# Kernel tuning notes

Measured on AMD Instinct MI355X. Metric: run time of the kernel, lower is better.

## Reference

```python
import jax, jax.numpy as jnp
import numpy as np

R = 3           # disp_range = (3, 3)
DU = 2 * R + 1  # 7 displacements per axis, 49 total
PNAMES = ['mn_w1','mn_b1','mn_w2','mn_b2','mn_w3','mn_b3','mn_w4','mn_b4','mn_wd','mn_bd','mn_w5','mn_b5','dap_w','dap_b','me_w1','me_b1','me_w2','me_b2','me_w3','me_b3','gz1_w','gz1_b','gr1_w','gr1_b','gq1_w','gq1_b','gz2_w','gz2_b','gr2_w','gr2_b','gq2_w','gq2_b','fh_w1','fh_b1','fh_w2','fh_b2']


def conv2d(x, w, b, stride=(1, 1), padding=((1, 1), (1, 1))):
    y = jax.lax.conv_general_dilated(x, w, stride, padding, dimension_numbers=('NCHW', 'OIHW', 'NCHW'))
    return y + b[None, :, None, None]


def warp_backwards(f, flow):
    # bilinear backward warp with zero padding; flow[:,0]=u (x offset), flow[:,1]=v (y offset)
    B, C, H, W = f.shape
    gy, gx = jnp.meshgrid(jnp.arange(H, dtype=flow.dtype), jnp.arange(W, dtype=flow.dtype), indexing='ij')
    x = gx[None] + flow[:, 0]
    y = gy[None] + flow[:, 1]
    x0, y0 = jnp.floor(x), jnp.floor(y)
    wx, wy = x - x0, y - y0

    def corner(yy, xx, wgt):
        valid = (yy >= 0) & (yy <= H - 1) & (xx >= 0) & (xx <= W - 1)
        yc = jnp.clip(yy, 0, H - 1).astype(jnp.int32)
        xc = jnp.clip(xx, 0, W - 1).astype(jnp.int32)
        g = jax.vmap(lambda fb, yb, xb: fb[:, yb, xb])(f, yc, xc)  # (B,C,H,W)
        return g * (wgt * valid.astype(f.dtype))[:, None]

    return (corner(y0, x0, (1 - wy) * (1 - wx)) + corner(y0, x0 + 1, (1 - wy) * wx)
            + corner(y0 + 1, x0, wy * (1 - wx)) + corner(y0 + 1, x0 + 1, wy * wx))


def gru_step(h, x, wz, bz, wr, br, wq, bq, pad):
    hx = jnp.concatenate([h, x], axis=1)
    z = jax.nn.sigmoid(conv2d(hx, wz, bz, padding=pad))
    r = jax.nn.sigmoid(conv2d(hx, wr, br, padding=pad))
    q = jnp.tanh(conv2d(jnp.concatenate([r * h, x], axis=1), wq, bq, padding=pad))
    return (1.0 - z) * h + z * q


def _run(fmap1, fmap2, h, flow, P):
    B, C, H, W = fmap1.shape
    lrelu, relu = jax.nn.leaky_relu, jax.nn.relu
    # backward warp of fmap2 by current (detached) flow
    f2w = warp_backwards(fmap2, jax.lax.stop_gradient(flow))
    # --- correlation volume: 49 zero-padded shifts of warped fmap2, paired with fmap1 ---
    pad2 = jnp.pad(f2w, ((0, 0), (0, 0), (R, R), (R, R)))
    # k = i*DU + j  <->  shift (di, dj) = (i-R, j-R); shifted[...,y,x] = f2w[y+dj, x+di]
    shifted = jnp.stack([pad2[:, :, j:j + H, i:i + W] for i in range(DU) for j in range(DU)], axis=1)  # (B,49,C,H,W)
    valid = (jnp.sum(shifted, axis=2, keepdims=True) != 0).astype(fmap1.dtype)
    mvol = jnp.concatenate([jnp.broadcast_to(fmap1[:, None], shifted.shape), shifted], axis=2) * valid  # (B,49,2C,H,W)
    # --- matching net, applied per displacement ---
    x = mvol.reshape(B * DU * DU, 2 * C, H, W)
    x = relu(conv2d(x, P['mn_w1'], P['mn_b1']))
    x = relu(conv2d(x, P['mn_w2'], P['mn_b2'], stride=(2, 2)))
    x = relu(conv2d(x, P['mn_w3'], P['mn_b3']))
    x = relu(conv2d(x, P['mn_w4'], P['mn_b4']))
    # ConvTranspose2d(k=4, s=2, p=1) == lhs-dilated conv with pad 2
    x = jax.lax.conv_general_dilated(x, P['mn_wd'], (1, 1), ((2, 2), (2, 2)), lhs_dilation=(2, 2), dimension_numbers=('NCHW', 'OIHW', 'NCHW')) + P['mn_bd'][None, :, None, None]
    x = relu(x)
    x = conv2d(x, P['mn_w5'], P['mn_b5'])  # (B*49, 1, H, W)
    cvol = x.reshape(B, DU * DU, H, W)
    # --- displacement-aware projection: 1x1 conv across the 49 displacement channels ---
    cvol = jnp.einsum('ok,bkhw->bohw', P['dap_w'], cvol) + P['dap_b'][None, :, None, None]
    # --- motion encoder ---
    m = jnp.concatenate([cvol, fmap1, flow], axis=1)  # (B, 49+C+2, H, W)
    m = lrelu(conv2d(m, P['me_w1'], P['me_b1']))
    m = lrelu(conv2d(m, P['me_w2'], P['me_b2']))
    m = conv2d(m, P['me_w3'], P['me_b3'])             # (B, 94, H, W)
    xg = jnp.concatenate([m, flow], axis=1)           # (B, 96, H, W)
    # --- separable conv GRU: horizontal (1x5) then vertical (5x1) pass ---
    h = gru_step(h, xg, P['gz1_w'], P['gz1_b'], P['gr1_w'], P['gr1_b'], P['gq1_w'], P['gq1_b'], ((0, 0), (2, 2)))
    h = gru_step(h, xg, P['gz2_w'], P['gz2_b'], P['gr2_w'], P['gr2_b'], P['gq2_w'], P['gq2_b'], ((2, 2), (0, 0)))
    # --- flow head: softmax over 49 displacements, expectation of displacement grid ---
    s = lrelu(jnp.einsum('oi,bihw->bohw', P['fh_w1'], h) + P['fh_b1'][None, :, None, None])
    s = lrelu(jnp.einsum('oi,bihw->bohw', P['fh_w2'], s) + P['fh_b2'][None, :, None, None])
    prob = jax.nn.softmax(s, axis=1)  # (B, 49, H, W)
    dr = jnp.arange(-R, R + 1, dtype=fmap1.dtype)
    disp = jnp.stack([jnp.broadcast_to(dr[:, None], (DU, DU)), jnp.broadcast_to(dr[None, :], (DU, DU))], axis=0).reshape(2, DU * DU)
    d = jnp.einsum('bkhw,ck->bchw', prob, disp)
    return h, flow + d


def _params(key):
    shapes = {'mn_w1': (96, 64, 3, 3), 'mn_b1': (96,), 'mn_w2': (128, 96, 3, 3), 'mn_b2': (128,), 'mn_w3': (128, 128, 3, 3), 'mn_b3': (128,), 'mn_w4': (64, 128, 3, 3), 'mn_b4': (64,), 'mn_wd': (32, 64, 4, 4), 'mn_bd': (32,), 'mn_w5': (1, 32, 3, 3), 'mn_b5': (1,), 'dap_w': (49, 49), 'dap_b': (49,), 'me_w1': (128, 83, 3, 3), 'me_b1': (128,), 'me_w2': (128, 128, 3, 3), 'me_b2': (128,), 'me_w3': (94, 128, 3, 3), 'me_b3': (94,), 'gz1_w': (128, 224, 1, 5), 'gz1_b': (128,), 'gr1_w': (128, 224, 1, 5), 'gr1_b': (128,), 'gq1_w': (128, 224, 1, 5), 'gq1_b': (128,), 'gz2_w': (128, 224, 5, 1), 'gz2_b': (128,), 'gr2_w': (128, 224, 5, 1), 'gr2_b': (128,), 'gq2_w': (128, 224, 5, 1), 'gq2_b': (128,), 'fh_w1': (256, 128), 'fh_b1': (256,), 'fh_w2': (49, 256), 'fh_b2': (49,)}
    keys = jax.random.split(key, len(shapes))
    return {n: jax.random.normal(k, s, dtype=jnp.float32) * 0.05 for (n, s), k in zip(shapes.items(), keys)}


def setup_inputs():
    key = jax.random.key(0)
    k1, k2, k3, k4, kp = jax.random.split(key, 5)
    B, C, H, W, HID = 2, 32, 64, 96, 128
    inp = {'fmap1': jax.random.normal(k1, (B, C, H, W), jnp.float32),
           'fmap2': jax.random.normal(k2, (B, C, H, W), jnp.float32),
           'h': jax.random.normal(k3, (B, HID, H, W), jnp.float32),
           'flow': jax.random.normal(k4, (B, 2, H, W), jnp.float32),
           'i': 0}
    inp.update(_params(kp))
    return inp


def reference(fmap1, fmap2, h, flow, mn_w1, mn_b1, mn_w2, mn_b2, mn_w3, mn_b3, mn_w4, mn_b4, mn_wd, mn_bd, mn_w5, mn_b5, dap_w, dap_b, me_w1, me_b1, me_w2, me_b2, me_w3, me_b3, gz1_w, gz1_b, gr1_w, gr1_b, gq1_w, gq1_b, gz2_w, gz2_b, gr2_w, gr2_b, gq2_w, gq2_b, fh_w1, fh_b1, fh_w2, fh_b2, i):
    ps = (mn_w1, mn_b1, mn_w2, mn_b2, mn_w3, mn_b3, mn_w4, mn_b4, mn_wd, mn_bd, mn_w5, mn_b5, dap_w, dap_b, me_w1, me_b1, me_w2, me_b2, me_w3, me_b3, gz1_w, gz1_b, gr1_w, gr1_b, gq1_w, gq1_b, gz2_w, gz2_b, gr2_w, gr2_b, gq2_w, gq2_b, fh_w1, fh_b1, fh_w2, fh_b2)
    return _run(fmap1, fmap2, h, flow, dict(zip(PNAMES, ps)))
```

## Files before the change

kernel.cpp:

```cpp
#include <hip/hip_runtime.h>
#include <math.h>

typedef unsigned short u16;
typedef unsigned int u32;
typedef __attribute__((ext_vector_type(8))) short bf16x8;
typedef __attribute__((ext_vector_type(4))) float f32x4;

#define HWW 6144

__device__ __forceinline__ float sigmoidf_(float x) { return 1.f / (1.f + expf(-x)); }
__device__ __forceinline__ float lrelu_(float x) { return x >= 0.f ? x : 0.01f * x; }
__device__ __forceinline__ u16 f2bf(float f) {
    u32 u = __float_as_uint(f);
    u += 0x7fffu + ((u >> 16) & 1u);
    return (u16)(u >> 16);
}
__device__ __forceinline__ float bf2f(u16 h) { return __uint_as_float(((u32)h) << 16); }
__device__ __forceinline__ u32 pk2(float a, float b) { return (u32)f2bf(a) | ((u32)f2bf(b) << 16); }

struct WJob { const float* src; unsigned long dstOff; int OC, rowOff, IC, ICP, NT; unsigned long cum; };
struct WJobs { WJob j[16]; long total; };

__global__ __launch_bounds__(256) void k_wt_all(WJobs J, u16* __restrict__ base)
{
    long i = (long)blockIdx.x * 256 + threadIdx.x;
    if (i >= J.total) return;
    int jb = 0;
    #pragma unroll
    for (int k = 1; k < 16; ++k) if (i >= (long)J.j[k].cum) jb = k;
    WJob w = J.j[jb];
    long local = i - (long)w.cum;
    int c = (int)(local % w.ICP);
    int t = (int)((local / w.ICP) % w.NT);
    int o = (int)(local / ((long)w.ICP * w.NT));
    float val = (c < w.IC) ? w.src[((long)o * w.IC + c) * w.NT + t] : 0.f;
    base[w.dstOff + ((long)(w.rowOff + o) * w.NT + t) * w.ICP + c] = f2bf(val);
}

__global__ __launch_bounds__(256) void k_wt_dq(const float* __restrict__ w, u16* __restrict__ dst)
{
    int i = blockIdx.x * 256 + threadIdx.x;
    if (i >= 32768) return;
    int c = i & 63; int t = (i >> 6) & 3; int o = (i >> 8) & 31; int q = i >> 13;
    int ry = q >> 1, rx = q & 1, ta = t >> 1, tb = t & 1;
    int ky = ry + 2 * ta, kx = rx + 2 * tb;
    float val = w[(((long)o * 64 + c) * 4 + ky) * 4 + kx];
    dst[(long)q * 8192 + o * 256 + t * 64 + c] = f2bf(val);
}

__global__ __launch_bounds__(256) void k_wt5(const float* __restrict__ w, float* __restrict__ wt)
{
    int i = blockIdx.x * 256 + threadIdx.x;
    if (i >= 288) return;
    int t = i % 9, c = i / 9;
    wt[t * 32 + c] = w[c * 9 + t];
}

__global__ void k_catb(const float* __restrict__ a, const float* __restrict__ b, float* __restrict__ d)
{
    int i = threadIdx.x;
    if (i < 128) d[i] = a[i];
    else if (i < 256) d[i] = b[i - 128];
}

__global__ __launch_bounds__(256) void k_prep_f1(const float* __restrict__ fmap1, u16* __restrict__ f1bf)
{
    int gid = blockIdx.x * 256 + threadIdx.x;
    if (gid >= 24576) return;
    int idx = gid >> 1, half = gid & 1;
    int b = idx / HWW, p = idx % HWW;
    const float* fb = fmap1 + (long)b * 32 * HWW + p + (long)(half * 16) * HWW;
    u32 pk[8];
    #pragma unroll
    for (int c2 = 0; c2 < 8; ++c2)
        pk[c2] = pk2(fb[(long)(2 * c2) * HWW], fb[(long)(2 * c2 + 1) * HWW]);
    u16* op = f1bf + ((long)idx << 5) + half * 16;
    ((uint4*)op)[0] = make_uint4(pk[0], pk[1], pk[2], pk[3]);
    ((uint4*)op)[1] = make_uint4(pk[4], pk[5], pk[6], pk[7]);
}

__global__ __launch_bounds__(256) void k_warp(const float* __restrict__ fmap2, const float* __restrict__ flow,
                                              u16* __restrict__ f2wbf, float* __restrict__ cs)
{
    int gid = blockIdx.x * 256 + threadIdx.x;
    if (gid >= 24576) return;
    int idx = gid >> 1, half = gid & 1;
    int b = idx / HWW, p = idx % HWW, y = p / 96, x = p % 96;
    float u = flow[(b * 2 + 0) * HWW + p], v = flow[(b * 2 + 1) * HWW + p];
    float fx = (float)x + u, fy = (float)y + v;
    float fx0 = floorf(fx), fy0 = floorf(fy);
    float wx = fx - fx0, wy = fy - fy0;
    int x0 = (int)fx0, y0i = (int)fy0, x1 = x0 + 1, y1 = y0i + 1;
    bool vx0 = x0 >= 0 && x0 < 96, vx1 = x1 >= 0 && x1 < 96;
    bool vy0 = y0i >= 0 && y0i < 64, vy1 = y1 >= 0 && y1 < 64;
    float m00 = (vy0 && vx0) ? (1.f - wy) * (1.f - wx) : 0.f;
    float m01 = (vy0 && vx1) ? (1.f - wy) * wx : 0.f;
    float m10 = (vy1 && vx0) ? wy * (1.f - wx) : 0.f;
    float m11 = (vy1 && vx1) ? wy * wx : 0.f;
    int cx0 = min(max(x0, 0), 95), cx1 = min(max(x1, 0), 95);
    int cy0 = min(max(y0i, 0), 63), cy1 = min(max(y1, 0), 63);
    int i00 = cy0 * 96 + cx0, i01 = cy0 * 96 + cx1, i10 = cy1 * 96 + cx0, i11 = cy1 * 96 + cx1;
    const float* fb = fmap2 + (long)b * 32 * HWW + (long)(half * 16) * HWW;
    float s = 0.f; u32 pk[8];
    #pragma unroll
    for (int c2 = 0; c2 < 8; ++c2) {
        const float* fa = fb + (long)(2 * c2) * HWW;
        const float* fc = fb + (long)(2 * c2 + 1) * HWW;
        float g0 = m00 * fa[i00] + m01 * fa[i01] + m10 * fa[i10] + m11 * fa[i11];
        float g1 = m00 * fc[i00] + m01 * fc[i01] + m10 * fc[i10] + m11 * fc[i11];
        s += g0 + g1;
        pk[c2] = pk2(g0, g1);
    }
    u16* op = f2wbf + ((long)idx << 5) + half * 16;
    ((uint4*)op)[0] = make_uint4(pk[0], pk[1], pk[2], pk[3]);
    ((uint4*)op)[1] = make_uint4(pk[4], pk[5], pk[6], pk[7]);
    float stot = s + __shfl_xor(s, 1);
    if (half == 0) cs[idx] = stot;
}

template<int BN, int MODE, int KH, int KW, int PH, int PW, int STRIDE, int ACT, int OUTF32,
         int IH, int IW, int OH, int OW, int ICP, int NKT>
__global__ __launch_bounds__(256) void k_gemm(
    const u16* __restrict__ A0, const u16* __restrict__ A1,
    const float* __restrict__ csm, const u16* __restrict__ Wb,
    const float* __restrict__ bias,
    u16* __restrict__ outb, u16* __restrict__ outb2, float* __restrict__ outf,
    int OC, int ldc, int coff, int nOff)
{
    constexpr int WAVES_M = (BN == 128) ? 2 : 4;
    constexpr int WTM = 128 / WAVES_M;
    constexpr int WTN = (BN == 128) ? 64 : BN;
    constexpr int MF = WTM / 16;
    constexpr int NF = WTN / 16;
    constexpr int LDR = 40;
    __shared__ u16 As[2][128 * LDR];
    __shared__ u16 Bs[2][BN * LDR];
    int tid = threadIdx.x;
    int mrow = tid >> 1;
    int khOff = (tid & 1) << 4;
    int gmS = blockIdx.x * 128 + mrow;

    constexpr int OHW = (MODE == 1) ? 6144 : ((MODE == 2) ? 1536 : OH * OW);
    constexpr int OWW = (MODE == 1) ? 96 : ((MODE == 2) ? 48 : OW);
    int nImg = gmS / OHW;
    int rem = gmS - nImg * OHW;
    int y0 = rem / OWW, x0 = rem - y0 * OWW;

    int ryz = 0, rxz = 0, diS = 0, djS = 0, bImgHWW = 0;
    u32 vmask = 0;
    const u16* Arow = A0;
    if (MODE == 0) {
        Arow = A0 + ((long)nImg * IH * IW + (long)y0 * STRIDE * IW + (long)x0 * STRIDE) * ICP + khOff;
    } else if (MODE == 1) {
        int n = nOff + nImg;
        int bImg = n / 49; int kd = n - bImg * 49;
        diS = kd / 7 - 3; djS = kd % 7 - 3;
        bImgHWW = bImg * HWW;
        #pragma unroll
        for (int t = 0; t < 9; ++t) {
            int dy = t / 3 - 1, dx = t % 3 - 1;
            int yy = y0 + dy, xx = x0 + dx, ys = yy + djS, xs = xx + diS;
            bool v = yy >= 0 && yy < 64 && xx >= 0 && xx < 96 && ys >= 0 && ys < 64 && xs >= 0 && xs < 96;
            if (v) v = (csm[bImgHWW + ys * 96 + xs] != 0.f);
            vmask |= (v ? 1u : 0u) << t;
        }
    } else {
        ryz = blockIdx.z >> 1; rxz = blockIdx.z & 1;
    }
    const u16* WbZ = Wb + (MODE == 2 ? (long)blockIdx.z * 32 * 256 : 0);
    int n0 = blockIdx.y * BN;

    auto loadTile = [&](int kt, uint4& va0, uint4& va1) {
        va0 = make_uint4(0u, 0u, 0u, 0u); va1 = make_uint4(0u, 0u, 0u, 0u);
        if (MODE == 0) {
            constexpr int KTC = ICP / 32;
            int t = kt / KTC;
            int c0 = (kt - t * KTC) << 5;
            int dy = t / KW - PH, dx = t - (t / KW) * KW - PW;
            int iy = y0 * STRIDE + dy, ix = x0 * STRIDE + dx;
            if (iy >= 0 && iy < IH && ix >= 0 && ix < IW) {
                const u16* sp = Arow + (long)(dy * IW + dx) * ICP + c0;
                va0 = *(const uint4*)sp; va1 = *(const uint4*)(sp + 8);
            }
        } else if (MODE == 1) {
            int t = kt >> 1, half = kt & 1;
            if ((vmask >> t) & 1u) {
                int dy = t / 3 - 1, dx = t % 3 - 1;
                int yy = y0 + dy, xx = x0 + dx;
                const u16* sp = half ? (A1 + (((long)bImgHWW + (yy + djS) * 96 + (xx + diS)) << 5) + khOff)
                                     : (A0 + (((long)bImgHWW + yy * 96 + xx) << 5) + khOff);
                va0 = *(const uint4*)sp; va1 = *(const uint4*)(sp + 8);
            }
        } else {
            int t = kt >> 1, c0 = (kt & 1) << 5;
            int ta = t >> 1, tb = t & 1;
            int iy = y0 + ryz + ta - 1, ix = x0 + rxz + tb - 1;
            if (iy >= 0 && iy < 32 && ix >= 0 && ix < 48) {
                const u16* sp = A0 + (((long)(nImg * 32 + iy) * 48 + ix) << 6) + c0 + khOff;
                va0 = *(const uint4*)sp; va1 = *(const uint4*)(sp + 8);
            }
        }
    };

    int lane = tid & 63, wid = tid >> 6;
    int wm = (BN == 128) ? (wid >> 1) : wid;
    int wn = (BN == 128) ? (wid & 1) : 0;
    int fr = lane & 15, fg = lane >> 4;
    f32x4 acc[MF][NF];
    #pragma unroll
    for (int i = 0; i < MF; ++i)
        #pragma unroll
        for (int j = 0; j < NF; ++j)
            acc[i][j] = (f32x4){0.f, 0.f, 0.f, 0.f};

    bool bldr = (tid < 2 * BN);
    int brow = tid >> 1, ko = (tid & 1) << 4;
    const u16* Bp = WbZ + (long)(n0 + brow) * (NKT * 32) + ko;

    {
        uint4 a0c, a1c;
        loadTile(0, a0c, a1c);
        *(uint4*)&As[0][mrow * LDR + khOff] = a0c;
        *(uint4*)&As[0][mrow * LDR + khOff + 8] = a1c;
        if (bldr) {
            *(uint4*)&Bs[0][brow * LDR + ko] = *(const uint4*)Bp;
            *(uint4*)&Bs[0][brow * LDR + ko + 8] = *(const uint4*)(Bp + 8);
        }
    }
    __syncthreads();

    #pragma unroll
    for (int kt = 0; kt < NKT; ++kt) {
        constexpr int last = NKT - 1;
        int cur = kt & 1;
        uint4 na0, na1, nb0, nb1;
        if (kt < last) {
            loadTile(kt + 1, na0, na1);
            if (bldr) {
                const u16* wp = Bp + (long)(kt + 1) * 32;
                nb0 = *(const uint4*)wp; nb1 = *(const uint4*)(wp + 8);
            }
        }
        bf16x8 af[MF], bfv[NF];
        #pragma unroll
        for (int i = 0; i < MF; ++i)
            af[i] = *(const bf16x8*)&As[cur][(wm * WTM + i * 16 + fr) * LDR + fg * 8];
        #pragma unroll
        for (int j = 0; j < NF; ++j)
            bfv[j] = *(const bf16x8*)&Bs[cur][(wn * WTN + j * 16 + fr) * LDR + fg * 8];
        #pragma unroll
        for (int i = 0; i < MF; ++i)
            #pragma unroll
            for (int j = 0; j < NF; ++j)
                acc[i][j] = __builtin_amdgcn_mfma_f32_16x16x32_bf16(af[i], bfv[j], acc[i][j], 0, 0, 0);
        if (kt < last) {
            int bufn = cur ^ 1;
            *(uint4*)&As[bufn][mrow * LDR + khOff] = na0;
            *(uint4*)&As[bufn][mrow * LDR + khOff + 8] = na1;
            if (bldr) {
                *(uint4*)&Bs[bufn][brow * LDR + ko] = nb0;
                *(uint4*)&Bs[bufn][brow * LDR + ko + 8] = nb1;
            }
            __syncthreads();
        }
    }

    #pragma unroll
    for (int i = 0; i < MF; ++i) {
        #pragma unroll
        for (int j = 0; j < NF; ++j) {
            int nn = n0 + wn * WTN + j * 16 + fr;
            if (nn >= OC) continue;
            #pragma unroll
            for (int rr = 0; rr < 4; ++rr) {
                int mloc = wm * WTM + i * 16 + fg * 4 + rr;
                long gm = (long)blockIdx.x * 128 + mloc;
                float v = acc[i][j][rr] + bias[nn];
                if (ACT == 1) v = fmaxf(v, 0.f);
                else if (ACT == 2) v = lrelu_(v);
                if (OUTF32) {
                    outf[gm * ldc + coff + nn] = v;
                } else if (MODE == 2) {
                    int nI = (int)(gm / 1536); int rq = (int)(gm - (long)nI * 1536);
                    int Y = rq / 48, X = rq - (rq / 48) * 48;
                    long di = (((long)nI * 64 + 2 * Y + ryz) * 96 + (2 * X + rxz)) * 32 + nn;
                    outb[di] = f2bf(v);
                } else {
                    long di = gm * ldc + coff + nn;
                    u16 hv = f2bf(v);
                    outb[di] = hv;
                    if (outb2) outb2[di] = hv;
                }
            }
        }
    }
}

__global__ __launch_bounds__(256) void k_conv5n(const u16* __restrict__ x5, const float* __restrict__ w5t,
                                                const float* __restrict__ b5, u16* __restrict__ cvolT,
                                                int N, int n0)
{
    int idx = blockIdx.x * 256 + threadIdx.x;
    if (idx >= N * HWW) return;
    int nl = idx / HWW, p = idx % HWW, y = p / 96, x = p % 96;
    float acc = b5[0];
    #pragma unroll
    for (int t = 0; t < 9; ++t) {
        int iy = y + t / 3 - 1, ix = x + t % 3 - 1;
        if (iy < 0 || iy >= 64 || ix < 0 || ix >= 96) continue;
        const u16* sp = x5 + (((long)nl * HWW + iy * 96 + ix) << 5);
        const float* wt_ = w5t + t * 32;
        #pragma unroll
        for (int c8 = 0; c8 < 4; ++c8) {
            uint4 v = *(const uint4*)(sp + c8 * 8);
            acc = fmaf(bf2f((u16)(v.x & 0xffffu)), wt_[c8 * 8 + 0], acc);
            acc = fmaf(bf2f((u16)(v.x >> 16)),     wt_[c8 * 8 + 1], acc);
            acc = fmaf(bf2f((u16)(v.y & 0xffffu)), wt_[c8 * 8 + 2], acc);
            acc = fmaf(bf2f((u16)(v.y >> 16)),     wt_[c8 * 8 + 3], acc);
            acc = fmaf(bf2f((u16)(v.z & 0xffffu)), wt_[c8 * 8 + 4], acc);
            acc = fmaf(bf2f((u16)(v.z >> 16)),     wt_[c8 * 8 + 5], acc);
            acc = fmaf(bf2f((u16)(v.w & 0xffffu)), wt_[c8 * 8 + 6], acc);
            acc = fmaf(bf2f((u16)(v.w >> 16)),     wt_[c8 * 8 + 7], acc);
        }
    }
    int n = n0 + nl;
    int b = n / 49, k = n - b * 49;
    cvolT[((long)b * HWW + p) * 64 + k] = f2bf(acc);
}

__global__ __launch_bounds__(256) void k_me_tail(const float* __restrict__ fmap1, const float* __restrict__ flow,
                                                 u16* __restrict__ mein)
{
    int gid = blockIdx.x * 256 + threadIdx.x;
    if (gid >= 73728) return;
    int j = gid / 12288, idx = gid - j * 12288;
    int b = idx / HWW, p = idx % HWW;
    int c0 = 49 + j * 8;
    u16* mp = mein + (long)idx * 96;
    #pragma unroll
    for (int q = 0; q < 8; ++q) {
        int c = c0 + q;
        if (c >= 96) break;
        float v;
        if (c < 81) v = fmap1[((long)(b * 32 + (c - 49))) * HWW + p];
        else if (c == 81) v = flow[(b * 2 + 0) * HWW + p];
        else if (c == 82) v = flow[(b * 2 + 1) * HWW + p];
        else v = 0.f;
        mp[c] = f2bf(v);
    }
}

__global__ __launch_bounds__(256) void k_set_head(const float* __restrict__ h, const float* __restrict__ flow,
                                                  float* __restrict__ hst, u16* __restrict__ hx,
                                                  u16* __restrict__ hx2)
{
    int gid = blockIdx.x * 256 + threadIdx.x;
    if (gid >= 49152) return;
    int cq = gid / 12288, idx = gid - cq * 12288;
    int b = idx / HWW, p = idx % HWW;
    int c0 = cq * 32;
    const float* hp = h + (long)b * 128 * HWW + p;
    float* hs = hst + (long)idx * 128;
    u16* hxp = hx + (long)idx * 224;
    #pragma unroll
    for (int c = c0; c < c0 + 32; c += 8) {
        float v[8];
        #pragma unroll
        for (int q = 0; q < 8; ++q) v[q] = hp[(long)(c + q) * HWW];
        *(float4*)&hs[c] = make_float4(v[0], v[1], v[2], v[3]);
        *(float4*)&hs[c + 4] = make_float4(v[4], v[5], v[6], v[7]);
        uint4 pk = make_uint4(pk2(v[0], v[1]), pk2(v[2], v[3]), pk2(v[4], v[5]), pk2(v[6], v[7]));
        *(uint4*)&hxp[c] = pk;
    }
    if (cq == 0) {
        u16 uu = f2bf(flow[(b * 2 + 0) * HWW + p]);
        u16 vv = f2bf(flow[(b * 2 + 1) * HWW + p]);
        long o = (long)idx * 224;
        hx[o + 222] = uu; hx[o + 223] = vv;
        hx2[o + 222] = uu; hx2[o + 223] = vv;
    }
}

__global__ __launch_bounds__(256) void k_post_zr(const float* __restrict__ azr, const float* __restrict__ hst,
                                                 float* __restrict__ z, u16* __restrict__ hx2)
{
    int gid = blockIdx.x * 256 + threadIdx.x;
    if (gid >= 49152) return;
    int cq = gid / 12288, idx = gid - cq * 12288;
    int c0 = cq * 32;
    const float* ap = azr + (long)idx * 256;
    const float* hs = hst + (long)idx * 128;
    float* zp = z + (long)idx * 128;
    u16* xp = hx2 + (long)idx * 224;
    #pragma unroll
    for (int c = c0; c < c0 + 32; c += 8) {
        float4 a0 = *(const float4*)&ap[c], a1 = *(const float4*)&ap[c + 4];
        float4 r0 = *(const float4*)&ap[128 + c], r1 = *(const float4*)&ap[128 + c + 4];
        float4 h0 = *(const float4*)&hs[c], h1v = *(const float4*)&hs[c + 4];
        float z0 = sigmoidf_(a0.x), z1 = sigmoidf_(a0.y), z2 = sigmoidf_(a0.z), z3 = sigmoidf_(a0.w);
        float z4 = sigmoidf_(a1.x), z5 = sigmoidf_(a1.y), z6 = sigmoidf_(a1.z), z7 = sigmoidf_(a1.w);
        *(float4*)&zp[c] = make_float4(z0, z1, z2, z3);
        *(float4*)&zp[c + 4] = make_float4(z4, z5, z6, z7);
        float rh0 = sigmoidf_(r0.x) * h0.x, rh1 = sigmoidf_(r0.y) * h0.y;
        float rh2 = sigmoidf_(r0.z) * h0.z, rh3 = sigmoidf_(r0.w) * h0.w;
        float rh4 = sigmoidf_(r1.x) * h1v.x, rh5 = sigmoidf_(r1.y) * h1v.y;
        float rh6 = sigmoidf_(r1.z) * h1v.z, rh7 = sigmoidf_(r1.w) * h1v.w;
        uint4 pk = make_uint4(pk2(rh0, rh1), pk2(rh2, rh3), pk2(rh4, rh5), pk2(rh6, rh7));
        *(uint4*)&xp[c] = pk;
    }
}

template<int FIN>
__global__ __launch_bounds__(256) void k_post_q(const float* __restrict__ aq, const float* __restrict__ z,
                                                const float* __restrict__ hst, float* __restrict__ h1f,
                                                u16* __restrict__ hxdst, float* __restrict__ outH)
{
    int gid = blockIdx.x * 256 + threadIdx.x;
    if (gid >= 49152) return;
    int cq = gid / 12288, idx = gid - cq * 12288;
    int b = idx / HWW, p = idx % HWW;
    int c0 = cq * 32;
    const float* ap = aq + (long)idx * 128;
    const float* zp = z + (long)idx * 128;
    const float* hs = hst + (long)idx * 128;
    #pragma unroll
    for (int c = c0; c < c0 + 32; c += 8) {
        float hn[8];
        #pragma unroll
        for (int q = 0; q < 8; ++q) {
            float qq = tanhf(ap[c + q]);
            float zv = zp[c + q];
            hn[q] = (1.f - zv) * hs[c + q] + zv * qq;
        }
        uint4 pk = make_uint4(pk2(hn[0], hn[1]), pk2(hn[2], hn[3]), pk2(hn[4], hn[5]), pk2(hn[6], hn[7]));
        if (FIN == 0) {
            *(float4*)&h1f[(long)idx * 128 + c] = make_float4(hn[0], hn[1], hn[2], hn[3]);
            *(float4*)&h1f[(long)idx * 128 + c + 4] = make_float4(hn[4], hn[5], hn[6], hn[7]);
            *(uint4*)&hxdst[(long)idx * 224 + c] = pk;
        } else {
            #pragma unroll
            for (int q = 0; q < 8; ++q)
                outH[((long)(b * 128 + c + q)) * HWW + p] = hn[q];
            *(uint4*)&hxdst[(long)idx * 128 + c] = pk;
        }
    }
}

__global__ __launch_bounds__(256) void k_soft(const float* __restrict__ s2, const float* __restrict__ flow,
                                              float* __restrict__ outFlow)
{
    int idx = blockIdx.x * 256 + threadIdx.x;
    if (idx >= 12288) return;
    int b = idx / HWW, p = idx % HWW;
    const float* sp = s2 + (long)idx * 64;
    float lg[49];
    #pragma unroll
    for (int k = 0; k < 48; k += 4) {
        float4 v = *(const float4*)&sp[k];
        lg[k] = v.x; lg[k + 1] = v.y; lg[k + 2] = v.z; lg[k + 3] = v.w;
    }
    lg[48] = sp[48];
    float m = -1e30f;
    #pragma unroll
    for (int k = 0; k < 49; ++k) m = fmaxf(m, lg[k]);
    float s = 0.f, a0 = 0.f, a1 = 0.f;
    #pragma unroll
    for (int k = 0; k < 49; ++k) {
        float e = expf(lg[k] - m);
        s += e;
        a0 += e * (float)(k / 7 - 3);
        a1 += e * (float)(k % 7 - 3);
    }
    float inv = 1.f / s;
    outFlow[(long)(b * 2 + 0) * HWW + p] = flow[(long)(b * 2 + 0) * HWW + p] + a0 * inv;
    outFlow[(long)(b * 2 + 1) * HWW + p] = flow[(long)(b * 2 + 1) * HWW + p] + a1 * inv;
}

extern "C" void kernel_launch(void* const* d_in, const int* in_sizes, int n_in,
                              void* d_out, int out_size, void* d_ws, size_t ws_size,
                              hipStream_t stream)
{
    const float* fmap1 = (const float*)d_in[0];
    const float* fmap2 = (const float*)d_in[1];
    const float* h     = (const float*)d_in[2];
    const float* flow  = (const float*)d_in[3];
    int pb = (in_sizes[4] == 1) ? 5 : 4;
    const float* mn_w1 = (const float*)d_in[pb + 0];
    const float* mn_b1 = (const float*)d_in[pb + 1];
    const float* mn_w2 = (const float*)d_in[pb + 2];
    const float* mn_b2 = (const float*)d_in[pb + 3];
    const float* mn_w3 = (const float*)d_in[pb + 4];
    const float* mn_b3 = (const float*)d_in[pb + 5];
    const float* mn_w4 = (const float*)d_in[pb + 6];
    const float* mn_b4 = (const float*)d_in[pb + 7];
    const float* mn_wd = (const float*)d_in[pb + 8];
    const float* mn_bd = (const float*)d_in[pb + 9];
    const float* mn_w5 = (const float*)d_in[pb + 10];
    const float* mn_b5 = (const float*)d_in[pb + 11];
    const float* dap_w = (const float*)d_in[pb + 12];
    const float* dap_b = (const float*)d_in[pb + 13];
    const float* me_w1 = (const float*)d_in[pb + 14];
    const float* me_b1 = (const float*)d_in[pb + 15];
    const float* me_w2 = (const float*)d_in[pb + 16];
    const float* me_b2 = (const float*)d_in[pb + 17];
    const float* me_w3 = (const float*)d_in[pb + 18];
    const float* me_b3 = (const float*)d_in[pb + 19];
    const float* gz1_w = (const float*)d_in[pb + 20];
    const float* gz1_b = (const float*)d_in[pb + 21];
    const float* gr1_w = (const float*)d_in[pb + 22];
    const float* gr1_b = (const float*)d_in[pb + 23];
    const float* gq1_w = (const float*)d_in[pb + 24];
    const float* gq1_b = (const float*)d_in[pb + 25];
    const float* gz2_w = (const float*)d_in[pb + 26];
    const float* gz2_b = (const float*)d_in[pb + 27];
    const float* gr2_w = (const float*)d_in[pb + 28];
    const float* gr2_b = (const float*)d_in[pb + 29];
    const float* gq2_w = (const float*)d_in[pb + 30];
    const float* gq2_b = (const float*)d_in[pb + 31];
    const float* fh_w1 = (const float*)d_in[pb + 32];
    const float* fh_b1 = (const float*)d_in[pb + 33];
    const float* fh_w2 = (const float*)d_in[pb + 34];
    const float* fh_b2 = (const float*)d_in[pb + 35];

    char* wsB = (char*)d_ws;
    size_t off = 0;
    auto alc = [&](size_t bytes) { size_t o = off; off = (off + bytes + 255) & ~(size_t)255; return o; };

    size_t o_wc1  = alc(128 * 576 * 2);
    size_t o_wc2  = alc(128 * 864 * 2);
    size_t o_wc3  = alc((size_t)128 * 1152 * 2);
    size_t o_wc4  = alc((size_t)64 * 1152 * 2);
    size_t o_wdq  = alc(32768 * 2);
    size_t o_wme1 = alc(128 * 864 * 2);
    size_t o_wme2 = alc((size_t)128 * 1152 * 2);
    size_t o_wme3 = alc((size_t)128 * 1152 * 2);
    size_t o_wzr1 = alc((size_t)256 * 1120 * 2);
    size_t o_wq1  = alc((size_t)128 * 1120 * 2);
    size_t o_wzr2 = alc((size_t)256 * 1120 * 2);
    size_t o_wq2  = alc((size_t)128 * 1120 * 2);
    size_t o_wfh1 = alc(256 * 128 * 2);
    size_t o_wfh2 = alc(64 * 256 * 2);
    size_t o_wdapb= alc(64 * 64 * 2);
    size_t o_w5t  = alc(288 * 4);
    size_t o_bzr1 = alc(256 * 4);
    size_t o_bzr2 = alc(256 * 4);
    size_t wArenaBytes = off;

    size_t o_f1bf = alc((size_t)12288 * 32 * 2);
    size_t o_f2wb = alc((size_t)12288 * 32 * 2);
    size_t o_cs   = alc(12288 * 4);
    size_t o_cvolT= alc((size_t)12288 * 64 * 2);

    const int CH = 49;
    size_t sharedBase = off;
    size_t offA = sharedBase;
    auto alcA = [&](size_t bytes) { size_t o = offA; offA = (offA + bytes + 255) & ~(size_t)255; return o; };
    size_t o_x1 = alcA((size_t)CH * 6144 * 96 * 2);
    size_t o_x2 = alcA((size_t)98 * 1536 * 128 * 2);
    size_t o_x3 = alcA((size_t)98 * 1536 * 128 * 2);
    size_t o_x4 = alcA((size_t)98 * 1536 * 64 * 2);
    size_t o_x5 = alcA((size_t)98 * 6144 * 32 * 2);
    size_t offB2 = sharedBase;
    auto alcB = [&](size_t bytes) { size_t o = offB2; offB2 = (offB2 + bytes + 255) & ~(size_t)255; return o; };
    size_t o_mein = alcB((size_t)12288 * 96 * 2);
    size_t o_m1   = alcB((size_t)12288 * 128 * 2);
    size_t o_m2   = alcB((size_t)12288 * 128 * 2);
    size_t o_hx   = alcB((size_t)12288 * 224 * 2);
    size_t o_hx2  = alcB((size_t)12288 * 224 * 2);
    size_t o_h2bf = alcB((size_t)12288 * 128 * 2);
    size_t o_s1b  = alcB((size_t)12288 * 256 * 2);
    size_t o_hst  = alcB((size_t)12288 * 128 * 4);
    size_t o_h1f  = alcB((size_t)12288 * 128 * 4);
    size_t o_zf   = alcB((size_t)12288 * 128 * 4);
    size_t o_azr  = alcB((size_t)12288 * 256 * 4);
    size_t o_aqf  = alcB((size_t)12288 * 128 * 4);
    size_t o_s2   = alcB((size_t)12288 * 64 * 4);

    u16* wbase = (u16*)wsB;
    u16* wdq  = (u16*)(wsB + o_wdq);
    float* w5t = (float*)(wsB + o_w5t);
    float* bzr1 = (float*)(wsB + o_bzr1);
    float* bzr2 = (float*)(wsB + o_bzr2);
    u16* wc1  = (u16*)(wsB + o_wc1);   u16* wc2  = (u16*)(wsB + o_wc2);
    u16* wc3  = (u16*)(wsB + o_wc3);   u16* wc4  = (u16*)(wsB + o_wc4);
    u16* wme1 = (u16*)(wsB + o_wme1);  u16* wme2 = (u16*)(wsB + o_wme2);
    u16* wme3 = (u16*)(wsB + o_wme3);
    u16* wzr1 = (u16*)(wsB + o_wzr1);  u16* wq1  = (u16*)(wsB + o_wq1);
    u16* wzr2 = (u16*)(wsB + o_wzr2);  u16* wq2  = (u16*)(wsB + o_wq2);
    u16* wfh1 = (u16*)(wsB + o_wfh1);  u16* wfh2 = (u16*)(wsB + o_wfh2);
    u16* wdapb= (u16*)(wsB + o_wdapb);

    u16* f1bf = (u16*)(wsB + o_f1bf);  u16* f2wb = (u16*)(wsB + o_f2wb);
    float* cs = (float*)(wsB + o_cs);
    u16* cvolT = (u16*)(wsB + o_cvolT);
    u16* x1 = (u16*)(wsB + o_x1); u16* x2 = (u16*)(wsB + o_x2); u16* x3 = (u16*)(wsB + o_x3);
    u16* x4 = (u16*)(wsB + o_x4); u16* x5 = (u16*)(wsB + o_x5);
    u16* mein = (u16*)(wsB + o_mein);
    u16* m1 = (u16*)(wsB + o_m1); u16* m2 = (u16*)(wsB + o_m2);
    u16* hx = (u16*)(wsB + o_hx); u16* hx2 = (u16*)(wsB + o_hx2);
    u16* h2bf = (u16*)(wsB + o_h2bf);  u16* s1b = (u16*)(wsB + o_s1b);
    float* hst = (float*)(wsB + o_hst); float* h1f = (float*)(wsB + o_h1f);
    float* zf = (float*)(wsB + o_zf); float* azr = (float*)(wsB + o_azr);
    float* aqf = (float*)(wsB + o_aqf); float* s2 = (float*)(wsB + o_s2);

    float* outH = (float*)d_out;
    float* outFlow = outH + (long)2 * 128 * HWW;

    auto nb = [](long total, int bs) { return (unsigned)((total + bs - 1) / bs); };

    hipMemsetAsync(wsB, 0, wArenaBytes, stream);
    hipMemsetAsync(wsB + o_cvolT, 0, (size_t)12288 * 64 * 2, stream);

    WJobs J;
    {
        auto mk = [](const float* src, size_t dstOffBytes, int OC, int rowOff, int IC, int ICP, int NT) {
            WJob w; w.src = src; w.dstOff = dstOffBytes / 2; w.OC = OC; w.rowOff = rowOff;
            w.IC = IC; w.ICP = ICP; w.NT = NT; w.cum = 0; return w;
        };
        J.j[0]  = mk(mn_w1, o_wc1, 96, 0, 64, 64, 9);
        J.j[1]  = mk(mn_w2, o_wc2, 128, 0, 96, 96, 9);
        J.j[2]  = mk(mn_w3, o_wc3, 128, 0, 128, 128, 9);
        J.j[3]  = mk(mn_w4, o_wc4, 64, 0, 128, 128, 9);
        J.j[4]  = mk(me_w1, o_wme1, 128, 0, 83, 96, 9);
        J.j[5]  = mk(me_w2, o_wme2, 128, 0, 128, 128, 9);
        J.j[6]  = mk(me_w3, o_wme3, 94, 0, 128, 128, 9);
        J.j[7]  = mk(gz1_w, o_wzr1, 128, 0, 224, 224, 5);
        J.j[8]  = mk(gr1_w, o_wzr1, 128, 128, 224, 224, 5);
        J.j[9]  = mk(gq1_w, o_wq1, 128, 0, 224, 224, 5);
        J.j[10] = mk(gz2_w, o_wzr2, 128, 0, 224, 224, 5);
        J.j[11] = mk(gr2_w, o_wzr2, 128, 128, 224, 224, 5);
        J.j[12] = mk(gq2_w, o_wq2, 128, 0, 224, 224, 5);
        J.j[13] = mk(fh_w1, o_wfh1, 256, 0, 128, 128, 1);
        J.j[14] = mk(fh_w2, o_wfh2, 49, 0, 256, 256, 1);
        J.j[15] = mk(dap_w, o_wdapb, 49, 0, 49, 64, 1);
        long cum = 0;
        for (int k = 0; k < 16; ++k) {
            J.j[k].cum = cum;
            cum += (long)J.j[k].OC * J.j[k].NT * J.j[k].ICP;
        }
        J.total = cum;
    }
    k_wt_all<<<nb(J.total, 256), 256, 0, stream>>>(J, wbase);
    k_wt_dq<<<nb(32768, 256), 256, 0, stream>>>(mn_wd, wdq);
    k_wt5<<<2, 256, 0, stream>>>(mn_w5, w5t);
    k_catb<<<1, 256, 0, stream>>>(gz1_b, gr1_b, bzr1);
    k_catb<<<1, 256, 0, stream>>>(gz2_b, gr2_b, bzr2);

    k_prep_f1<<<nb(24576, 256), 256, 0, stream>>>(fmap1, f1bf);
    k_warp<<<nb(24576, 256), 256, 0, stream>>>(fmap2, flow, f2wb, cs);

    for (int n0 = 0; n0 < 98; n0 += CH) {
        k_gemm<128,1,3,3,1,1,1,1,0,64,96,64,96,32,18><<<dim3(2352, 1), 256, 0, stream>>>(
            f1bf, f2wb, cs, wc1, mn_b1, x1, nullptr, nullptr, 96, 96, 0, n0);
        k_gemm<128,0,3,3,1,1,2,1,0,64,96,32,48,96,27><<<dim3(588, 1), 256, 0, stream>>>(
            x1, nullptr, nullptr, wc2, mn_b2, x2 + (long)n0 * 196608, nullptr, nullptr, 128, 128, 0, 0);
    }
    k_gemm<128,0,3,3,1,1,1,1,0,32,48,32,48,128,36><<<dim3(1176, 1), 256, 0, stream>>>(
        x2, nullptr, nullptr, wc3, mn_b3, x3, nullptr, nullptr, 128, 128, 0, 0);
    k_gemm<64,0,3,3,1,1,1,1,0,32,48,32,48,128,36><<<dim3(1176, 1), 256, 0, stream>>>(
        x3, nullptr, nullptr, wc4, mn_b4, x4, nullptr, nullptr, 64, 64, 0, 0);
    k_gemm<32,2,4,4,2,2,1,1,0,32,48,32,48,64,8><<<dim3(1176, 1, 4), 256, 0, stream>>>(
        x4, nullptr, nullptr, wdq, mn_bd, x5, nullptr, nullptr, 32, 32, 0, 0);
    k_conv5n<<<nb(98L * HWW, 256), 256, 0, stream>>>(x5, w5t, mn_b5, cvolT, 98, 0);

    k_gemm<64,0,1,1,0,0,1,0,0,64,96,64,96,64,2><<<dim3(96, 1), 256, 0, stream>>>(
        cvolT, nullptr, nullptr, wdapb, dap_b, mein, nullptr, nullptr, 49, 96, 0, 0);
    k_me_tail<<<nb(73728, 256), 256, 0, stream>>>(fmap1, flow, mein);

    k_gemm<128,0,3,3,1,1,1,2,0,64,96,64,96,96,27><<<dim3(96, 1), 256, 0, stream>>>(
        mein, nullptr, nullptr, wme1, me_b1, m1, nullptr, nullptr, 128, 128, 0, 0);
    k_gemm<128,0,3,3,1,1,1,2,0,64,96,64,96,128,36><<<dim3(96, 1), 256, 0, stream>>>(
        m1, nullptr, nullptr, wme2, me_b2, m2, nullptr, nullptr, 128, 128, 0, 0);
    k_gemm<128,0,3,3,1,1,1,0,0,64,96,64,96,128,36><<<dim3(96, 1), 256, 0, stream>>>(
        m2, nullptr, nullptr, wme3, me_b3, hx, hx2, nullptr, 94, 224, 128, 0);

    k_set_head<<<nb(49152, 256), 256, 0, stream>>>(h, flow, hst, hx, hx2);
    k_gemm<128,0,1,5,0,2,1,0,1,64,96,64,96,224,35><<<dim3(96, 2), 256, 0, stream>>>(
        hx, nullptr, nullptr, wzr1, bzr1, nullptr, nullptr, azr, 256, 256, 0, 0);
    k_post_zr<<<nb(49152, 256), 256, 0, stream>>>(azr, hst, zf, hx2);
    k_gemm<128,0,1,5,0,2,1,0,1,64,96,64,96,224,35><<<dim3(96, 1), 256, 0, stream>>>(
        hx2, nullptr, nullptr, wq1, gq1_b, nullptr, nullptr, aqf, 128, 128, 0, 0);
    k_post_q<0><<<nb(49152, 256), 256, 0, stream>>>(aqf, zf, hst, h1f, hx, nullptr);

    k_gemm<128,0,5,1,2,0,1,0,1,64,96,64,96,224,35><<<dim3(96, 2), 256, 0, stream>>>(
        hx, nullptr, nullptr, wzr2, bzr2, nullptr, nullptr, azr, 256, 256, 0, 0);
    k_post_zr<<<nb(49152, 256), 256, 0, stream>>>(azr, h1f, zf, hx2);
    k_gemm<128,0,5,1,2,0,1,0,1,64,96,64,96,224,35><<<dim3(96, 1), 256, 0, stream>>>(
        hx2, nullptr, nullptr, wq2, gq2_b, nullptr, nullptr, aqf, 128, 128, 0, 0);
    k_post_q<1><<<nb(49152, 256), 256, 0, stream>>>(aqf, zf, h1f, nullptr, h2bf, outH);

    k_gemm<128,0,1,1,0,0,1,2,0,64,96,64,96,128,4><<<dim3(96, 2), 256, 0, stream>>>(
        h2bf, nullptr, nullptr, wfh1, fh_b1, s1b, nullptr, nullptr, 256, 256, 0, 0);
    k_gemm<64,0,1,1,0,0,1,2,1,64,96,64,96,256,8><<<dim3(96, 1), 256, 0, stream>>>(
        s1b, nullptr, nullptr, wfh2, fh_b2, nullptr, nullptr, s2, 49, 64, 0, 0);
    k_soft<<<nb(12288, 256), 256, 0, stream>>>(s2, flow, outFlow);
}
```

Baseline: 776.7 us.

## Add BM tile parameter and deepen global-load prefetch to two stages

Templates the GEMM kernel on the M tile size, so the small per-pixel convolutions in the motion encoder, GRU and flow head use 64-row tiles and launch twice as many blocks. It also restructures the main loop so global loads for tile k+2 are issued while tile k computes and tile k+1 is written to shared memory, hiding more load latency. The intent is better CU occupancy on the small launches and more latency hiding on all GEMMs. In exchange it holds extra prefetch registers per thread, which may reduce occupancy in the large correlation-stage GEMMs.

```diff
diff --git a/kernel.cpp b/kernel.cpp
--- a/kernel.cpp
+++ b/kernel.cpp
@@ -118,7 +118,7 @@
     if (half == 0) cs[idx] = stot;
 }
 
-template<int BN, int MODE, int KH, int KW, int PH, int PW, int STRIDE, int ACT, int OUTF32,
+template<int BM, int BN, int MODE, int KH, int KW, int PH, int PW, int STRIDE, int ACT, int OUTF32,
          int IH, int IW, int OH, int OW, int ICP, int NKT>
 __global__ __launch_bounds__(256) void k_gemm(
     const u16* __restrict__ A0, const u16* __restrict__ A1,
@@ -127,18 +127,20 @@
     u16* __restrict__ outb, u16* __restrict__ outb2, float* __restrict__ outf,
     int OC, int ldc, int coff, int nOff)
 {
-    constexpr int WAVES_M = (BN == 128) ? 2 : 4;
-    constexpr int WTM = 128 / WAVES_M;
-    constexpr int WTN = (BN == 128) ? 64 : BN;
+    constexpr int WAVES_M = (BM == 64) ? 2 : ((BN == 128) ? 2 : 4);
+    constexpr int WAVES_N = 4 / WAVES_M;
+    constexpr int WTM = BM / WAVES_M;
+    constexpr int WTN = BN / WAVES_N;
     constexpr int MF = WTM / 16;
     constexpr int NF = WTN / 16;
     constexpr int LDR = 40;
-    __shared__ u16 As[2][128 * LDR];
+    __shared__ u16 As[2][BM * LDR];
     __shared__ u16 Bs[2][BN * LDR];
     int tid = threadIdx.x;
-    int mrow = tid >> 1;
-    int khOff = (tid & 1) << 4;
-    int gmS = blockIdx.x * 128 + mrow;
+    constexpr int ATHR = 256 / BM;
+    int mrow = tid / ATHR;
+    int khOff = (tid % ATHR) * (32 / ATHR);
+    int gmS = blockIdx.x * BM + mrow;
 
     constexpr int OHW = (MODE == 1) ? 6144 : ((MODE == 2) ? 1536 : OH * OW);
     constexpr int OWW = (MODE == 1) ? 96 : ((MODE == 2) ? 48 : OW);
@@ -180,7 +182,8 @@
             int iy = y0 * STRIDE + dy, ix = x0 * STRIDE + dx;
             if (iy >= 0 && iy < IH && ix >= 0 && ix < IW) {
                 const u16* sp = Arow + (long)(dy * IW + dx) * ICP + c0;
-                va0 = *(const uint4*)sp; va1 = *(const uint4*)(sp + 8);
+                va0 = *(const uint4*)sp;
+                if (BM == 128) va1 = *(const uint4*)(sp + 8);
             }
         } else if (MODE == 1) {
             int t = kt >> 1, half = kt & 1;
@@ -189,7 +192,8 @@
                 int yy = y0 + dy, xx = x0 + dx;
                 const u16* sp = half ? (A1 + (((long)bImgHWW + (yy + djS) * 96 + (xx + diS)) << 5) + khOff)
                                      : (A0 + (((long)bImgHWW + yy * 96 + xx) << 5) + khOff);
-                va0 = *(const uint4*)sp; va1 = *(const uint4*)(sp + 8);
+                va0 = *(const uint4*)sp;
+                if (BM == 128) va1 = *(const uint4*)(sp + 8);
             }
         } else {
             int t = kt >> 1, c0 = (kt & 1) << 5;
@@ -197,49 +201,59 @@
             int iy = y0 + ryz + ta - 1, ix = x0 + rxz + tb - 1;
             if (iy >= 0 && iy < 32 && ix >= 0 && ix < 48) {
                 const u16* sp = A0 + (((long)(nImg * 32 + iy) * 48 + ix) << 6) + c0 + khOff;
-                va0 = *(const uint4*)sp; va1 = *(const uint4*)(sp + 8);
+                va0 = *(const uint4*)sp;
+                if (BM == 128) va1 = *(const uint4*)(sp + 8);
             }
         }
     };
-
-    int lane = tid & 63, wid = tid >> 6;
-    int wm = (BN == 128) ? (wid >> 1) : wid;
-    int wn = (BN == 128) ? (wid & 1) : 0;
-    int fr = lane & 15, fg = lane >> 4;
-    f32x4 acc[MF][NF];
-    #pragma unroll
-    for (int i = 0; i < MF; ++i)
-        #pragma unroll
-        for (int j = 0; j < NF; ++j)
-            acc[i][j] = (f32x4){0.f, 0.f, 0.f, 0.f};
+    auto writeA = [&](int bufn, const uint4& va0, const uint4& va1) {
+        *(uint4*)&As[bufn][mrow * LDR + khOff] = va0;
+        if (BM == 128) *(uint4*)&As[bufn][mrow * LDR + khOff + 8] = va1;
+    };
 
     bool bldr = (tid < 2 * BN);
     int brow = tid >> 1, ko = (tid & 1) << 4;
     const u16* Bp = WbZ + (long)(n0 + brow) * (NKT * 32) + ko;
-
+    auto loadB = [&](int kt, uint4& vb0, uint4& vb1) {
+        const u16* wp = Bp + (long)kt * 32;
+        vb0 = *(const uint4*)wp; vb1 = *(const uint4*)(wp + 8);
+    };
+    auto writeB = [&](int bufn, const uint4& vb0, const uint4& vb1) {
+        *(uint4*)&Bs[bufn][brow * LDR + ko] = vb0;
+        *(uint4*)&Bs[bufn][brow * LDR + ko + 8] = vb1;
+    };
+
+    int lane = tid & 63, wid = tid >> 6;
+    int wm = (WAVES_N == 2) ? (wid >> 1) : wid;
+    int wn = (WAVES_N == 2) ? (wid & 1) : 0;
+    int fr = lane & 15, fg = lane >> 4;
+    f32x4 acc[MF][NF];
+    #pragma unroll
+    for (int i = 0; i < MF; ++i)
+        #pragma unroll
+        for (int j = 0; j < NF; ++j)
+            acc[i][j] = (f32x4){0.f, 0.f, 0.f, 0.f};
+
+    uint4 pa0, pa1, pb0, pb1;
     {
-        uint4 a0c, a1c;
-        loadTile(0, a0c, a1c);
-        *(uint4*)&As[0][mrow * LDR + khOff] = a0c;
-        *(uint4*)&As[0][mrow * LDR + khOff + 8] = a1c;
-        if (bldr) {
-            *(uint4*)&Bs[0][brow * LDR + ko] = *(const uint4*)Bp;
-            *(uint4*)&Bs[0][brow * LDR + ko + 8] = *(const uint4*)(Bp + 8);
-        }
+        uint4 t0, t1;
+        loadTile(0, t0, t1);
+        writeA(0, t0, t1);
+        if (bldr) { uint4 u0, u1; loadB(0, u0, u1); writeB(0, u0, u1); }
+    }
+    if (NKT > 1) {
+        loadTile(1, pa0, pa1);
+        if (bldr) loadB(1, pb0, pb1);
     }
     __syncthreads();
 
     #pragma unroll
     for (int kt = 0; kt < NKT; ++kt) {
-        constexpr int last = NKT - 1;
         int cur = kt & 1;
-        uint4 na0, na1, nb0, nb1;
-        if (kt < last) {
-            loadTile(kt + 1, na0, na1);
-            if (bldr) {
-                const u16* wp = Bp + (long)(kt + 1) * 32;
-                nb0 = *(const uint4*)wp; nb1 = *(const uint4*)(wp + 8);
-            }
+        uint4 qa0, qa1, qb0, qb1;
+        if (kt + 2 < NKT) {
+            loadTile(kt + 2, qa0, qa1);
+            if (bldr) loadB(kt + 2, qb0, qb1);
         }
         bf16x8 af[MF], bfv[NF];
         #pragma unroll
@@ -253,15 +267,12 @@
             #pragma unroll
             for (int j = 0; j < NF; ++j)
                 acc[i][j] = __builtin_amdgcn_mfma_f32_16x16x32_bf16(af[i], bfv[j], acc[i][j], 0, 0, 0);
-        if (kt < last) {
+        if (kt + 1 < NKT) {
             int bufn = cur ^ 1;
-            *(uint4*)&As[bufn][mrow * LDR + khOff] = na0;
-            *(uint4*)&As[bufn][mrow * LDR + khOff + 8] = na1;
-            if (bldr) {
-                *(uint4*)&Bs[bufn][brow * LDR + ko] = nb0;
-                *(uint4*)&Bs[bufn][brow * LDR + ko + 8] = nb1;
-            }
+            writeA(bufn, pa0, pa1);
+            if (bldr) writeB(bufn, pb0, pb1);
             __syncthreads();
+            pa0 = qa0; pa1 = qa1; pb0 = qb0; pb1 = qb1;
         }
     }
 
@@ -274,7 +285,7 @@
             #pragma unroll
             for (int rr = 0; rr < 4; ++rr) {
                 int mloc = wm * WTM + i * 16 + fg * 4 + rr;
-                long gm = (long)blockIdx.x * 128 + mloc;
+                long gm = (long)blockIdx.x * BM + mloc;
                 float v = acc[i][j][rr] + bias[nn];
                 if (ACT == 1) v = fmaxf(v, 0.f);
                 else if (ACT == 2) v = lrelu_(v);
@@ -650,48 +661,48 @@
     k_warp<<<nb(24576, 256), 256, 0, stream>>>(fmap2, flow, f2wb, cs);
 
     for (int n0 = 0; n0 < 98; n0 += CH) {
-        k_gemm<128,1,3,3,1,1,1,1,0,64,96,64,96,32,18><<<dim3(2352, 1), 256, 0, stream>>>(
+        k_gemm<128,128,1,3,3,1,1,1,1,0,64,96,64,96,32,18><<<dim3(2352, 1), 256, 0, stream>>>(
             f1bf, f2wb, cs, wc1, mn_b1, x1, nullptr, nullptr, 96, 96, 0, n0);
-        k_gemm<128,0,3,3,1,1,2,1,0,64,96,32,48,96,27><<<dim3(588, 1), 256, 0, stream>>>(
+        k_gemm<128,128,0,3,3,1,1,2,1,0,64,96,32,48,96,27><<<dim3(588, 1), 256, 0, stream>>>(
             x1, nullptr, nullptr, wc2, mn_b2, x2 + (long)n0 * 196608, nullptr, nullptr, 128, 128, 0, 0);
     }
-    k_gemm<128,0,3,3,1,1,1,1,0,32,48,32,48,128,36><<<dim3(1176, 1), 256, 0, stream>>>(
+    k_gemm<128,128,0,3,3,1,1,1,1,0,32,48,32,48,128,36><<<dim3(1176, 1), 256, 0, stream>>>(
         x2, nullptr, nullptr, wc3, mn_b3, x3, nullptr, nullptr, 128, 128, 0, 0);
-    k_gemm<64,0,3,3,1,1,1,1,0,32,48,32,48,128,36><<<dim3(1176, 1), 256, 0, stream>>>(
+    k_gemm<128,64,0,3,3,1,1,1,1,0,32,48,32,48,128,36><<<dim3(1176, 1), 256, 0, stream>>>(
         x3, nullptr, nullptr, wc4, mn_b4, x4, nullptr, nullptr, 64, 64, 0, 0);
-    k_gemm<32,2,4,4,2,2,1,1,0,32,48,32,48,64,8><<<dim3(1176, 1, 4), 256, 0, stream>>>(
+    k_gemm<128,32,2,4,4,2,2,1,1,0,32,48,32,48,64,8><<<dim3(1176, 1, 4), 256, 0, stream>>>(
         x4, nullptr, nullptr, wdq, mn_bd, x5, nullptr, nullptr, 32, 32, 0, 0);
     k_conv5n<<<nb(98L * HWW, 256), 256, 0, stream>>>(x5, w5t, mn_b5, cvolT, 98, 0);
 
-    k_gemm<64,0,1,1,0,0,1,0,0,64,96,64,96,64,2><<<dim3(96, 1), 256, 0, stream>>>(
+    k_gemm<64,64,0,1,1,0,0,1,0,0,64,96,64,96,64,2><<<dim3(192, 1), 256, 0, stream>>>(
         cvolT, nullptr, nullptr, wdapb, dap_b, mein, nullptr, nullptr, 49, 96, 0, 0);
     k_me_tail<<<nb(73728, 256), 256, 0, stream>>>(fmap1, flow, mein);
 
-    k_gemm<128,0,3,3,1,1,1,2,0,64,96,64,96,96,27><<<dim3(96, 1), 256, 0, stream>>>(
+    k_gemm<64,128,0,3,3,1,1,1,2,0,64,96,64,96,96,27><<<dim3(192, 1), 256, 0, stream>>>(
         mein, nullptr, nullptr, wme1, me_b1, m1, nullptr, nullptr, 128, 128, 0, 0);
-    k_gemm<128,0,3,3,1,1,1,2,0,64,96,64,96,128,36><<<dim3(96, 1), 256, 0, stream>>>(
+    k_gemm<64,128,0,3,3,1,1,1,2,0,64,96,64,96,128,36><<<dim3(192, 1), 256, 0, stream>>>(
         m1, nullptr, nullptr, wme2, me_b2, m2, nullptr, nullptr, 128, 128, 0, 0);
-    k_gemm<128,0,3,3,1,1,1,0,0,64,96,64,96,128,36><<<dim3(96, 1), 256, 0, stream>>>(
+    k_gemm<64,128,0,3,3,1,1,1,0,0,64,96,64,96,128,36><<<dim3(192, 1), 256, 0, stream>>>(
         m2, nullptr, nullptr, wme3, me_b3, hx, hx2, nullptr, 94, 224, 128, 0);
 
     k_set_head<<<nb(49152, 256), 256, 0, stream>>>(h, flow, hst, hx, hx2);
-    k_gemm<128,0,1,5,0,2,1,0,1,64,96,64,96,224,35><<<dim3(96, 2), 256, 0, stream>>>(
+    k_gemm<64,128,0,1,5,0,2,1,0,1,64,96,64,96,224,35><<<dim3(192, 2), 256, 0, stream>>>(
         hx, nullptr, nullptr, wzr1, bzr1, nullptr, nullptr, azr, 256, 256, 0, 0);
     k_post_zr<<<nb(49152, 256), 256, 0, stream>>>(azr, hst, zf, hx2);
-    k_gemm<128,0,1,5,0,2,1,0,1,64,96,64,96,224,35><<<dim3(96, 1), 256, 0, stream>>>(
+    k_gemm<64,128,0,1,5,0,2,1,0,1,64,96,64,96,224,35><<<dim3(192, 1), 256, 0, stream>>>(
         hx2, nullptr, nullptr, wq1, gq1_b, nullptr, nullptr, aqf, 128, 128, 0, 0);
     k_post_q<0><<<nb(49152, 256), 256, 0, stream>>>(aqf, zf, hst, h1f, hx, nullptr);
 
-    k_gemm<128,0,5,1,2,0,1,0,1,64,96,64,96,224,35><<<dim3(96, 2), 256, 0, stream>>>(
+    k_gemm<64,128,0,5,1,2,0,1,0,1,64,96,64,96,224,35><<<dim3(192, 2), 256, 0, stream>>>(
         hx, nullptr, nullptr, wzr2, bzr2, nullptr, nullptr, azr, 256, 256, 0, 0);
     k_post_zr<<<nb(49152, 256), 256, 0, stream>>>(azr, h1f, zf, hx2);
-    k_gemm<128,0,5,1,2,0,1,0,1,64,96,64,96,224,35><<<dim3(96, 1), 256, 0, stream>>>(
+    k_gemm<64,128,0,5,1,2,0,1,0,1,64,96,64,96,224,35><<<dim3(192, 1), 256, 0, stream>>>(
         hx2, nullptr, nullptr, wq2, gq2_b, nullptr, nullptr, aqf, 128, 128, 0, 0);
     k_post_q<1><<<nb(49152, 256), 256, 0, stream>>>(aqf, zf, h1f, nullptr, h2bf, outH);
 
-    k_gemm<128,0,1,1,0,0,1,2,0,64,96,64,96,128,4><<<dim3(96, 2), 256, 0, stream>>>(
+    k_gemm<64,128,0,1,1,0,0,1,2,0,64,96,64,96,128,4><<<dim3(192, 2), 256, 0, stream>>>(
         h2bf, nullptr, nullptr, wfh1, fh_b1, s1b, nullptr, nullptr, 256, 256, 0, 0);
-    k_gemm<64,0,1,1,0,0,1,2,1,64,96,64,96,256,8><<<dim3(96, 1), 256, 0, stream>>>(
+    k_gemm<64,64,0,1,1,0,0,1,2,1,64,96,64,96,256,8><<<dim3(192, 1), 256, 0, stream>>>(
         s1b, nullptr, nullptr, wfh2, fh_b2, nullptr, nullptr, s2, 49, 64, 0, 0);
     k_soft<<<nb(12288, 256), 256, 0, stream>>>(s2, flow, outFlow);
 }
```

Result: faster. 761.0 us (-2.0%).
